# Optimization experiments

Hardware: AMD Instinct MI355X
Metric: run time of the kernel (lower is better)

Reference implementation:

```python
import jax, jax.numpy as jnp
import numpy as np

N, K, D, VOCAB = 20000, 32, 128, 100000
NEG = -1e30  # finite large-negative so all-masked rows don't produce NaN softmax


def setup_inputs() -> dict:
    key = jax.random.key(0)
    ks = jax.random.split(key, 10)
    return {
        "nodes": jax.random.randint(ks[0], (N,), 0, VOCAB),
        "neigh_idx": jax.random.randint(ks[1], (N, K), 0, VOCAB),
        "neigh_len": jax.random.randint(ks[2], (N,), 0, K + 1),
        "u2e": jax.random.normal(ks[3], (VOCAB, D), dtype=jnp.float32),
        "W1": jax.random.normal(ks[4], (D, 2 * D), dtype=jnp.float32) * 0.05,
        "b1": jax.random.normal(ks[5], (D,), dtype=jnp.float32) * 0.05,
        "W2": jax.random.normal(ks[6], (D, D), dtype=jnp.float32) * 0.05,
        "b2": jax.random.normal(ks[7], (D,), dtype=jnp.float32) * 0.05,
        "W3": jax.random.normal(ks[8], (1, D), dtype=jnp.float32) * 0.05,
        "b3": jax.random.normal(ks[9], (1,), dtype=jnp.float32) * 0.05,
    }


def reference(nodes, neigh_idx, neigh_len, u2e, W1, b1, W2, b2, W3, b3):
    # self features: [N, D]
    self_feats = u2e[nodes]
    # neighbor features gather: [N, K, D]
    e_u = u2e[neigh_idx]
    # GraphRec Attention: cat(neighbor, self-broadcast) -> MLP -> softmax over K
    x = jnp.concatenate(
        [e_u, jnp.broadcast_to(self_feats[:, None, :], e_u.shape)], axis=-1
    )  # [N, K, 2D]
    h = jax.nn.relu(jnp.einsum("nkf,df->nkd", x, W1) + b1)
    h = jax.nn.relu(jnp.einsum("nkd,ed->nke", h, W2) + b2)
    logits = jnp.einsum("nkd,od->nko", h, W3)[..., 0] + b3[0]  # [N, K]
    mask = jnp.arange(K)[None, :] < neigh_len[:, None]  # [N, K]
    att = jax.nn.softmax(jnp.where(mask, logits, NEG), axis=1)
    att = jnp.where(mask, att, 0.0)  # zero out padded slots (and all-empty rows)
    # attention-weighted neighbor aggregation: [N, D]
    agg = jnp.einsum("nk,nkd->nd", att, e_u)
    has_neigh = (neigh_len > 0)[:, None]
    return jnp.where(has_neigh, (agg + self_feats) * 0.5, self_feats)
```

## Files before the change

kernel.cpp:

```cpp
#include <hip/hip_runtime.h>
#include <hip/hip_bf16.h>
#include <stdint.h>

#define KN 32
#define D  128
#define NNODES 20000
#define GRID 2500
#define ITERS 4
#define VOCAB 100000
#define CONV_BLOCKS (VOCAB * D / 2048)

typedef __bf16 bf16;
typedef __bf16 bf16x8 __attribute__((ext_vector_type(8)));
typedef float  f32x4  __attribute__((ext_vector_type(4)));

#define CHUNK_E 520
#define EU_NODE_E (8 * CHUNK_E)
#define H_STRIDE 136

#define GL2LDS(src, dst) __builtin_amdgcn_global_load_lds(                 \
    (const __attribute__((address_space(1))) void*)(src),                  \
    (__attribute__((address_space(3))) void*)(dst), 16, 0, 0)

#define MFMA(a, b, c) __builtin_amdgcn_mfma_f32_16x16x32_bf16((a), (b), (c), 0, 0, 0)

__global__ __launch_bounds__(256) void pack_weights_kernel(
    const float* __restrict__ W1, const float* __restrict__ W2,
    bf16* __restrict__ w1p, bf16* __restrict__ w2p)
{
    int t = blockIdx.x * 256 + threadIdx.x;
    if (t < 32768) {
        int j = t & 7, lane = (t >> 3) & 63, kt = (t >> 9) & 7, nt = t >> 12;
        int d = nt * 16 + (lane & 15);
        int f = kt * 32 + ((lane >> 4) << 3) + j;
        w1p[t] = (bf16)W1[d * 256 + f];
    } else if (t < 49152) {
        int u = t - 32768;
        int j = u & 7, lane = (u >> 3) & 63, kt = (u >> 9) & 3, nt = u >> 11;
        int e  = nt * 16 + (lane & 15);
        int dd = kt * 32 + ((lane >> 4) << 3) + j;
        w2p[u] = (bf16)W2[e * 128 + dd];
    }
}

__global__ __launch_bounds__(256) void prep_kernel(
    const float* __restrict__ u2e, const float* __restrict__ W1,
    const float* __restrict__ W2,
    bf16* __restrict__ tbl, bf16* __restrict__ w1p, bf16* __restrict__ w2p)
{
    int b = blockIdx.x;
    if (b < CONV_BLOCKS) {
        size_t i = ((size_t)b * 256 + threadIdx.x) * 8;
        float4 a = *(const float4*)(u2e + i);
        float4 c = *(const float4*)(u2e + i + 4);
        bf16x8 v;
        v[0]=(bf16)a.x; v[1]=(bf16)a.y; v[2]=(bf16)a.z; v[3]=(bf16)a.w;
        v[4]=(bf16)c.x; v[5]=(bf16)c.y; v[6]=(bf16)c.z; v[7]=(bf16)c.w;
        *(bf16x8*)(tbl + i) = v;
    } else {
        int t = (b - CONV_BLOCKS) * 256 + threadIdx.x;
        if (t < 32768) {
            int j = t & 7, lane = (t >> 3) & 63, kt = (t >> 9) & 7, nt = t >> 12;
            int d = nt * 16 + (lane & 15);
            int f = kt * 32 + ((lane >> 4) << 3) + j;
            w1p[t] = (bf16)W1[d * 256 + f];
        } else if (t < 49152) {
            int u = t - 32768;
            int j = u & 7, lane = (u >> 3) & 63, kt = (u >> 9) & 3, nt = u >> 11;
            int e  = nt * 16 + (lane & 15);
            int dd = kt * 32 + ((lane >> 4) << 3) + j;
            w2p[u] = (bf16)W2[e * 128 + dd];
        }
    }
}

__global__ __launch_bounds__(256, 4) void graphrec_agg_kernel(
    const int*   __restrict__ nodes,
    const int*   __restrict__ neigh_idx,
    const int*   __restrict__ neigh_len,
    const float* __restrict__ u2e,
    const bf16*  __restrict__ u2e_bf,
    const float* __restrict__ b1,
    const float* __restrict__ b2,
    const float* __restrict__ W3,
    const float* __restrict__ b3,
    const bf16*  __restrict__ w1p,
    const bf16*  __restrict__ w2p,
    float*       __restrict__ out)
{
    __shared__ alignas(16) bf16  eu[2 * EU_NODE_E];
    __shared__ alignas(16) float self_f[2 * D];
    __shared__ alignas(16) bf16  h1[2 * KN * H_STRIDE];
    __shared__ float lpart[2][4 * KN];

    const int t    = threadIdx.x;
    const int lane = t & 63;
    const int wave = t >> 6;
    const int ln15 = lane & 15;
    const int quad = lane >> 4;
    const int nt0  = wave * 2;

    const float bias1_0 = b1[nt0 * 16 + ln15];
    const float bias1_1 = b1[(nt0 + 1) * 16 + ln15];
    const float bias2_0 = b2[nt0 * 16 + ln15];
    const float bias2_1 = b2[(nt0 + 1) * 16 + ln15];
    const float w3_0    = W3[nt0 * 16 + ln15];
    const float w3_1    = W3[(nt0 + 1) * 16 + ln15];
    const float b3v     = b3[0];

    f32x4 cs0 = {0.f,0.f,0.f,0.f}, cs1 = cs0;
    {
        int nid = nodes[blockIdx.x * 8 + (ln15 & 7)];
        #pragma unroll
        for (int kt = 0; kt < 4; ++kt) {
            bf16x8 a   = *(const bf16x8*)(u2e_bf + (size_t)nid * D + kt * 32 + quad * 8);
            bf16x8 bb0 = *(const bf16x8*)(w1p + (nt0 * 8 + 4 + kt) * 512 + lane * 8);
            bf16x8 bb1 = *(const bf16x8*)(w1p + ((nt0 + 1) * 8 + 4 + kt) * 512 + lane * 8);
            cs0 = MFMA(a, bb0, cs0);
            cs1 = MFMA(a, bb1, cs1);
        }
    }

    bf16x8 w1r[2][4];
    #pragma unroll
    for (int nt = 0; nt < 2; ++nt)
        #pragma unroll
        for (int ft = 0; ft < 4; ++ft)
            w1r[nt][ft] = *(const bf16x8*)(w1p + ((nt0 + nt) * 8 + ft) * 512 + lane * 8);
    bf16x8 w2r[2][4];
    #pragma unroll
    for (int nt = 0; nt < 2; ++nt)
        #pragma unroll
        for (int kt = 0; kt < 4; ++kt)
            w2r[nt][kt] = *(const bf16x8*)(w2p + ((nt0 + nt) * 4 + kt) * 512 + lane * 8);

    #pragma unroll 1
    for (int it = 0; it < ITERS; ++it) {
        const int nA   = blockIdx.x * 8 + it * 2;
        const int lenA = neigh_len[nA];
        const int lenB = neigh_len[nA + 1];

        {
            const int gnd = wave >> 1;
            const int cb  = (wave & 1) * 4;
            #pragma unroll
            for (int j = 0; j < 4; ++j) {
                int chunk = cb + j;
                int idx = neigh_idx[(nA + gnd) * KN + chunk + ((lane >> 4) << 3)];
                GL2LDS(u2e_bf + (size_t)idx * D + ((lane & 15) << 3),
                       eu + gnd * EU_NODE_E + chunk * CHUNK_E);
            }
            if (wave == 0) {
                int sidx = nodes[nA + (lane >> 5)];
                GL2LDS(u2e + (size_t)sidx * D + ((lane & 31) << 2), self_f);
            }
        }
        __syncthreads();

        const bool hi = (it & 1);
        const float selA0 = hi ? cs0[2] : cs0[0];
        const float selB0 = hi ? cs0[3] : cs0[1];
        const float selA1 = hi ? cs1[2] : cs1[0];
        const float selB1 = hi ? cs1[3] : cs1[1];
        const int   srcl  = ((it >> 1) << 4) + ln15;
        const float svA0 = __shfl(selA0, srcl);
        const float svB0 = __shfl(selB0, srcl);
        const float svA1 = __shfl(selA1, srcl);
        const float svB1 = __shfl(selB1, srcl);

        #pragma unroll 1
        for (int nd = 0; nd < 2; ++nd) {
            const bf16* euN = eu + nd * EU_NODE_E;
            bf16* h1N = h1 + nd * KN * H_STRIDE;

            f32x4 c00 = {0.f,0.f,0.f,0.f}, c01 = c00, c10 = c00, c11 = c00;
            const int rb = (ln15 & 7) * CHUNK_E + (ln15 >> 3) * 128;
            #pragma unroll
            for (int ft = 0; ft < 4; ++ft) {
                bf16x8 a0 = *(const bf16x8*)(euN + rb + ft * 32 + quad * 8);
                bf16x8 a1 = *(const bf16x8*)(euN + rb + 256 + ft * 32 + quad * 8);
                c00 = MFMA(a0, w1r[0][ft], c00);
                c01 = MFMA(a0, w1r[1][ft], c01);
                c10 = MFMA(a1, w1r[0][ft], c10);
                c11 = MFMA(a1, w1r[1][ft], c11);
            }
            const float s0 = nd ? svB0 : svA0;
            const float s1 = nd ? svB1 : svA1;
            #pragma unroll
            for (int r = 0; r < 4; ++r) {
                int row = quad * 4 + r;
                h1N[row * H_STRIDE + nt0 * 16 + ln15]              = (bf16)fmaxf(c00[r] + bias1_0 + s0, 0.f);
                h1N[row * H_STRIDE + (nt0 + 1) * 16 + ln15]        = (bf16)fmaxf(c01[r] + bias1_1 + s1, 0.f);
                h1N[(16 + row) * H_STRIDE + nt0 * 16 + ln15]       = (bf16)fmaxf(c10[r] + bias1_0 + s0, 0.f);
                h1N[(16 + row) * H_STRIDE + (nt0 + 1) * 16 + ln15] = (bf16)fmaxf(c11[r] + bias1_1 + s1, 0.f);
            }
        }
        __syncthreads();

        #pragma unroll 1
        for (int nd = 0; nd < 2; ++nd) {
            const bf16* h1N = h1 + nd * KN * H_STRIDE;
            f32x4 d00 = {0.f,0.f,0.f,0.f}, d01 = d00, d10 = d00, d11 = d00;
            #pragma unroll
            for (int kt = 0; kt < 4; ++kt) {
                bf16x8 a0 = *(const bf16x8*)(h1N + ln15 * H_STRIDE + kt * 32 + quad * 8);
                bf16x8 a1 = *(const bf16x8*)(h1N + (16 + ln15) * H_STRIDE + kt * 32 + quad * 8);
                d00 = MFMA(a0, w2r[0][kt], d00);
                d01 = MFMA(a0, w2r[1][kt], d01);
                d10 = MFMA(a1, w2r[0][kt], d10);
                d11 = MFMA(a1, w2r[1][kt], d11);
            }
            #pragma unroll
            for (int r = 0; r < 4; ++r) {
                float p0 = w3_0 * fmaxf(d00[r] + bias2_0, 0.f)
                         + w3_1 * fmaxf(d01[r] + bias2_1, 0.f);
                float p1 = w3_0 * fmaxf(d10[r] + bias2_0, 0.f)
                         + w3_1 * fmaxf(d11[r] + bias2_1, 0.f);
                #pragma unroll
                for (int o = 1; o < 16; o <<= 1) {
                    p0 += __shfl_xor(p0, o);
                    p1 += __shfl_xor(p1, o);
                }
                if (ln15 == 0) {
                    lpart[nd][wave * KN + quad * 4 + r]      = p0;
                    lpart[nd][wave * KN + 16 + quad * 4 + r] = p1;
                }
            }
        }
        __syncthreads();

        {
            const int nd = wave >> 1;
            const int k  = lane & 31;
            float lg = lpart[nd][k] + lpart[nd][KN + k] + lpart[nd][2 * KN + k]
                     + lpart[nd][3 * KN + k] + b3v;
            const int len = nd ? lenB : lenA;
            bool act = k < len;
            float l = act ? lg : -1e30f;
            float m = l;
            #pragma unroll
            for (int o = 1; o < 32; o <<= 1) m = fmaxf(m, __shfl_xor(m, o));
            float e = act ? expf(l - m) : 0.f;
            float s = e;
            #pragma unroll
            for (int o = 1; o < 32; o <<= 1) s += __shfl_xor(s, o);
            float att = (s > 0.f) ? (e / s) : 0.f;

            const int d = ((wave & 1) << 6) + lane;
            const bf16* euN = eu + nd * EU_NODE_E;
            float acc = 0.f;
            #pragma unroll
            for (int k2 = 0; k2 < KN; ++k2) {
                float a  = __shfl(att, k2);
                float ev = (float)euN[(k2 & 7) * CHUNK_E + (k2 >> 3) * 128 + (d & 127)];
                acc += a * ev;
            }
            float sf = self_f[nd * D + (d & 127)];
            out[(size_t)(nA + nd) * D + (d & 127)] = (len > 0) ? 0.5f * (acc + sf) : sf;
        }
        __syncthreads();
    }
}

#define FB_CHUNK_DW 260
#define FB_EU_NODE_DW (16 * FB_CHUNK_DW)

__global__ __launch_bounds__(256, 3) void graphrec_agg_fb(
    const int*   __restrict__ nodes,
    const int*   __restrict__ neigh_idx,
    const int*   __restrict__ neigh_len,
    const float* __restrict__ u2e,
    const float* __restrict__ b1,
    const float* __restrict__ b2,
    const float* __restrict__ W3,
    const float* __restrict__ b3,
    const bf16*  __restrict__ w1p,
    const bf16*  __restrict__ w2p,
    float*       __restrict__ out)
{
    __shared__ alignas(16) float eu[2 * FB_EU_NODE_DW];
    __shared__ alignas(16) bf16  h1[2 * KN * H_STRIDE];
    __shared__ alignas(16) float self_f[2 * D];
    __shared__ float lpart[2][4 * KN];
    __shared__ float att_s[2][KN];

    const int t    = threadIdx.x;
    const int lane = t & 63;
    const int wave = t >> 6;
    const int ln15 = lane & 15;
    const int quad = lane >> 4;
    const int nt0  = wave * 2;

    const float bias1_0 = b1[nt0 * 16 + ln15];
    const float bias1_1 = b1[(nt0 + 1) * 16 + ln15];
    const float bias2_0 = b2[nt0 * 16 + ln15];
    const float bias2_1 = b2[(nt0 + 1) * 16 + ln15];
    const float w3_0    = W3[nt0 * 16 + ln15];
    const float w3_1    = W3[(nt0 + 1) * 16 + ln15];
    const float b3v     = b3[0];

    bf16x8 w1r[2][8];
    #pragma unroll
    for (int nt = 0; nt < 2; ++nt)
        #pragma unroll
        for (int ft = 0; ft < 8; ++ft)
            w1r[nt][ft] = *(const bf16x8*)(w1p + ((nt0 + nt) * 8 + ft) * 512 + lane * 8);
    bf16x8 w2r[2][4];
    #pragma unroll
    for (int nt = 0; nt < 2; ++nt)
        #pragma unroll
        for (int kt = 0; kt < 4; ++kt)
            w2r[nt][kt] = *(const bf16x8*)(w2p + ((nt0 + nt) * 4 + kt) * 512 + lane * 8);

    #pragma unroll 1
    for (int it = 0; it < 4; ++it) {
        const int nA   = blockIdx.x * 8 + it * 2;
        const int lenA = neigh_len[nA];
        const int lenB = neigh_len[nA + 1];
        {
            const int half = lane >> 5;
            const int colb = (lane & 31) << 4;
            #pragma unroll
            for (int nd = 0; nd < 2; ++nd) {
                #pragma unroll
                for (int j = 0; j < 4; ++j) {
                    int chunk = wave * 4 + j;
                    int idx = neigh_idx[(nA + nd) * KN + chunk + (half << 4)];
                    const char* src = (const char*)(u2e + (size_t)idx * D) + colb;
                    GL2LDS(src, eu + nd * FB_EU_NODE_DW + chunk * FB_CHUNK_DW);
                }
            }
            if (wave == 0) {
                int sidx = nodes[nA + half];
                const char* src = (const char*)(u2e + (size_t)sidx * D) + colb;
                GL2LDS(src, self_f);
            }
        }
        __syncthreads();
        #pragma unroll 1
        for (int nd = 0; nd < 2; ++nd) {
            const float* euN = eu + nd * FB_EU_NODE_DW;
            const float* sfN = self_f + nd * D;
            bf16* h1N = h1 + nd * KN * H_STRIDE;
            f32x4 c00 = {0.f,0.f,0.f,0.f}, c01 = c00, c10 = c00, c11 = c00;
            const int r0 = ln15 * FB_CHUNK_DW;
            #pragma unroll
            for (int ft = 0; ft < 4; ++ft) {
                int off = ft * 32 + quad * 8;
                f32x4 u0 = *(const f32x4*)(euN + r0 + off);
                f32x4 u1 = *(const f32x4*)(euN + r0 + off + 4);
                f32x4 v0 = *(const f32x4*)(euN + r0 + 128 + off);
                f32x4 v1 = *(const f32x4*)(euN + r0 + 128 + off + 4);
                bf16x8 a0, a1;
                #pragma unroll
                for (int e = 0; e < 4; ++e) {
                    a0[e] = (bf16)u0[e]; a0[4 + e] = (bf16)u1[e];
                    a1[e] = (bf16)v0[e]; a1[4 + e] = (bf16)v1[e];
                }
                c00 = MFMA(a0, w1r[0][ft], c00);
                c01 = MFMA(a0, w1r[1][ft], c01);
                c10 = MFMA(a1, w1r[0][ft], c10);
                c11 = MFMA(a1, w1r[1][ft], c11);
            }
            #pragma unroll
            for (int ft = 4; ft < 8; ++ft) {
                int off = (ft - 4) * 32 + quad * 8;
                f32x4 u0 = *(const f32x4*)(sfN + off);
                f32x4 u1 = *(const f32x4*)(sfN + off + 4);
                bf16x8 a;
                #pragma unroll
                for (int e = 0; e < 4; ++e) { a[e] = (bf16)u0[e]; a[4 + e] = (bf16)u1[e]; }
                c00 = MFMA(a, w1r[0][ft], c00);
                c01 = MFMA(a, w1r[1][ft], c01);
                c10 = MFMA(a, w1r[0][ft], c10);
                c11 = MFMA(a, w1r[1][ft], c11);
            }
            #pragma unroll
            for (int r = 0; r < 4; ++r) {
                int row = quad * 4 + r;
                h1N[row * H_STRIDE + nt0 * 16 + ln15]              = (bf16)fmaxf(c00[r] + bias1_0, 0.f);
                h1N[row * H_STRIDE + (nt0 + 1) * 16 + ln15]        = (bf16)fmaxf(c01[r] + bias1_1, 0.f);
                h1N[(16 + row) * H_STRIDE + nt0 * 16 + ln15]       = (bf16)fmaxf(c10[r] + bias1_0, 0.f);
                h1N[(16 + row) * H_STRIDE + (nt0 + 1) * 16 + ln15] = (bf16)fmaxf(c11[r] + bias1_1, 0.f);
            }
        }
        __syncthreads();
        #pragma unroll 1
        for (int nd = 0; nd < 2; ++nd) {
            const bf16* h1N = h1 + nd * KN * H_STRIDE;
            f32x4 d00 = {0.f,0.f,0.f,0.f}, d01 = d00, d10 = d00, d11 = d00;
            #pragma unroll
            for (int kt = 0; kt < 4; ++kt) {
                bf16x8 a0 = *(const bf16x8*)(h1N + ln15 * H_STRIDE + kt * 32 + quad * 8);
                bf16x8 a1 = *(const bf16x8*)(h1N + (16 + ln15) * H_STRIDE + kt * 32 + quad * 8);
                d00 = MFMA(a0, w2r[0][kt], d00);
                d01 = MFMA(a0, w2r[1][kt], d01);
                d10 = MFMA(a1, w2r[0][kt], d10);
                d11 = MFMA(a1, w2r[1][kt], d11);
            }
            #pragma unroll
            for (int r = 0; r < 4; ++r) {
                float p0 = w3_0 * fmaxf(d00[r] + bias2_0, 0.f)
                         + w3_1 * fmaxf(d01[r] + bias2_1, 0.f);
                float p1 = w3_0 * fmaxf(d10[r] + bias2_0, 0.f)
                         + w3_1 * fmaxf(d11[r] + bias2_1, 0.f);
                #pragma unroll
                for (int o = 1; o < 16; o <<= 1) {
                    p0 += __shfl_xor(p0, o);
                    p1 += __shfl_xor(p1, o);
                }
                if (ln15 == 0) {
                    lpart[nd][wave * KN + quad * 4 + r]      = p0;
                    lpart[nd][wave * KN + 16 + quad * 4 + r] = p1;
                }
            }
        }
        __syncthreads();
        if (wave < 2) {
            int nd = wave, k = lane & 31;
            float lg = lpart[nd][k] + lpart[nd][KN + k] + lpart[nd][2 * KN + k]
                     + lpart[nd][3 * KN + k] + b3v;
            int len = nd ? lenB : lenA;
            bool act = (lane < 32) && (k < len);
            float l = act ? lg : -1e30f;
            float m = l;
            #pragma unroll
            for (int o = 1; o < 32; o <<= 1) m = fmaxf(m, __shfl_xor(m, o));
            float e = act ? expf(l - m) : 0.f;
            float s = e;
            #pragma unroll
            for (int o = 1; o < 32; o <<= 1) s += __shfl_xor(s, o);
            if (lane < 32) att_s[nd][k] = (s > 0.f) ? (e / s) : 0.f;
        }
        __syncthreads();
        {
            int nd = t >> 7, d = t & 127;
            const float* euN = eu + nd * FB_EU_NODE_DW;
            float acc = 0.f;
            #pragma unroll
            for (int k = 0; k < KN; ++k)
                acc += att_s[nd][k] * euN[(k & 15) * FB_CHUNK_DW + ((k >> 4) << 7) + d];
            float sf = self_f[nd * D + d];
            int len = nd ? lenB : lenA;
            out[(size_t)(nA + nd) * D + d] = (len > 0) ? 0.5f * (acc + sf) : sf;
        }
        __syncthreads();
    }
}

extern "C" void kernel_launch(void* const* d_in, const int* in_sizes, int n_in,
                              void* d_out, int out_size, void* d_ws, size_t ws_size,
                              hipStream_t stream) {
    const int*   nodes     = (const int*)d_in[0];
    const int*   neigh_idx = (const int*)d_in[1];
    const int*   neigh_len = (const int*)d_in[2];
    const float* u2e       = (const float*)d_in[3];
    const float* W1        = (const float*)d_in[4];
    const float* b1        = (const float*)d_in[5];
    const float* W2        = (const float*)d_in[6];
    const float* b2        = (const float*)d_in[7];
    const float* W3        = (const float*)d_in[8];
    const float* b3        = (const float*)d_in[9];
    float* out = (float*)d_out;

    bf16*  w1p    = (bf16*)d_ws;
    bf16*  w2p    = w1p + 32768;
    bf16*  u2e_bf = (bf16*)((char*)d_ws + 98304);
    const size_t need = 98304ull + (size_t)VOCAB * D * 2;

    if (ws_size >= need) {
        prep_kernel<<<CONV_BLOCKS + 192, 256, 0, stream>>>(u2e, W1, W2,
                                                           u2e_bf, w1p, w2p);
        graphrec_agg_kernel<<<GRID, 256, 0, stream>>>(nodes, neigh_idx, neigh_len,
                                                      u2e, u2e_bf, b1, b2,
                                                      W3, b3, w1p, w2p, out);
    } else {
        pack_weights_kernel<<<192, 256, 0, stream>>>(W1, W2, w1p, w2p);
        graphrec_agg_fb<<<GRID, 256, 0, stream>>>(nodes, neigh_idx, neigh_len, u2e,
                                                  b1, b2, W3, b3, w1p, w2p, out);
    }
}
```

Before: 216.1 us.

## Drop bf16 table prep pass; gather fp32 rows and convert inline

Removes the prep kernel that converted the whole 100000x128 embedding table to bf16 and repacked the weights each call. The main kernel now gathers fp32 neighbor rows into registers, converts them to bf16 and writes them to LDS, and builds weight fragments straight from fp32 W1/W2. This avoids reading and writing the full table when only about 640K rows are gathered. The cost is twice the bytes per gathered row, register staging instead of direct global-to-LDS loads, and per-block weight conversion.

```diff
diff --git a/kernel.cpp b/kernel.cpp
--- a/kernel.cpp
+++ b/kernel.cpp
@@ -8,7 +8,6 @@
 #define GRID 2500
 #define ITERS 4
 #define VOCAB 100000
-#define CONV_BLOCKS (VOCAB * D / 2048)
 
 typedef __bf16 bf16;
 typedef __bf16 bf16x8 __attribute__((ext_vector_type(8)));
@@ -24,54 +23,13 @@
 
 #define MFMA(a, b, c) __builtin_amdgcn_mfma_f32_16x16x32_bf16((a), (b), (c), 0, 0, 0)
 
-__global__ __launch_bounds__(256) void pack_weights_kernel(
-    const float* __restrict__ W1, const float* __restrict__ W2,
-    bf16* __restrict__ w1p, bf16* __restrict__ w2p)
-{
-    int t = blockIdx.x * 256 + threadIdx.x;
-    if (t < 32768) {
-        int j = t & 7, lane = (t >> 3) & 63, kt = (t >> 9) & 7, nt = t >> 12;
-        int d = nt * 16 + (lane & 15);
-        int f = kt * 32 + ((lane >> 4) << 3) + j;
-        w1p[t] = (bf16)W1[d * 256 + f];
-    } else if (t < 49152) {
-        int u = t - 32768;
-        int j = u & 7, lane = (u >> 3) & 63, kt = (u >> 9) & 3, nt = u >> 11;
-        int e  = nt * 16 + (lane & 15);
-        int dd = kt * 32 + ((lane >> 4) << 3) + j;
-        w2p[u] = (bf16)W2[e * 128 + dd];
-    }
-}
-
-__global__ __launch_bounds__(256) void prep_kernel(
-    const float* __restrict__ u2e, const float* __restrict__ W1,
-    const float* __restrict__ W2,
-    bf16* __restrict__ tbl, bf16* __restrict__ w1p, bf16* __restrict__ w2p)
-{
-    int b = blockIdx.x;
-    if (b < CONV_BLOCKS) {
-        size_t i = ((size_t)b * 256 + threadIdx.x) * 8;
-        float4 a = *(const float4*)(u2e + i);
-        float4 c = *(const float4*)(u2e + i + 4);
-        bf16x8 v;
-        v[0]=(bf16)a.x; v[1]=(bf16)a.y; v[2]=(bf16)a.z; v[3]=(bf16)a.w;
-        v[4]=(bf16)c.x; v[5]=(bf16)c.y; v[6]=(bf16)c.z; v[7]=(bf16)c.w;
-        *(bf16x8*)(tbl + i) = v;
-    } else {
-        int t = (b - CONV_BLOCKS) * 256 + threadIdx.x;
-        if (t < 32768) {
-            int j = t & 7, lane = (t >> 3) & 63, kt = (t >> 9) & 7, nt = t >> 12;
-            int d = nt * 16 + (lane & 15);
-            int f = kt * 32 + ((lane >> 4) << 3) + j;
-            w1p[t] = (bf16)W1[d * 256 + f];
-        } else if (t < 49152) {
-            int u = t - 32768;
-            int j = u & 7, lane = (u >> 3) & 63, kt = (u >> 9) & 3, nt = u >> 11;
-            int e  = nt * 16 + (lane & 15);
-            int dd = kt * 32 + ((lane >> 4) << 3) + j;
-            w2p[u] = (bf16)W2[e * 128 + dd];
-        }
-    }
+__device__ __forceinline__ bf16x8 frag_from_f32(const float* __restrict__ p) {
+    float4 u0 = *(const float4*)(p);
+    float4 u1 = *(const float4*)(p + 4);
+    bf16x8 a;
+    a[0]=(bf16)u0.x; a[1]=(bf16)u0.y; a[2]=(bf16)u0.z; a[3]=(bf16)u0.w;
+    a[4]=(bf16)u1.x; a[5]=(bf16)u1.y; a[6]=(bf16)u1.z; a[7]=(bf16)u1.w;
+    return a;
 }
 
 __global__ __launch_bounds__(256, 4) void graphrec_agg_kernel(
@@ -79,13 +37,12 @@
     const int*   __restrict__ neigh_idx,
     const int*   __restrict__ neigh_len,
     const float* __restrict__ u2e,
-    const bf16*  __restrict__ u2e_bf,
+    const float* __restrict__ W1,
     const float* __restrict__ b1,
+    const float* __restrict__ W2,
     const float* __restrict__ b2,
     const float* __restrict__ W3,
     const float* __restrict__ b3,
-    const bf16*  __restrict__ w1p,
-    const bf16*  __restrict__ w2p,
     float*       __restrict__ out)
 {
     __shared__ alignas(16) bf16  eu[2 * EU_NODE_E];
@@ -108,31 +65,33 @@
     const float w3_1    = W3[(nt0 + 1) * 16 + ln15];
     const float b3v     = b3[0];
 
+    const size_t w1rowA = (size_t)(nt0 * 16 + ln15) * 256;
+    const size_t w1rowB = (size_t)((nt0 + 1) * 16 + ln15) * 256;
+    const size_t w2rowA = (size_t)(nt0 * 16 + ln15) * 128;
+    const size_t w2rowB = (size_t)((nt0 + 1) * 16 + ln15) * 128;
+    const int    kofs   = quad * 8;
+
     f32x4 cs0 = {0.f,0.f,0.f,0.f}, cs1 = cs0;
     {
         int nid = nodes[blockIdx.x * 8 + (ln15 & 7)];
         #pragma unroll
         for (int kt = 0; kt < 4; ++kt) {
-            bf16x8 a   = *(const bf16x8*)(u2e_bf + (size_t)nid * D + kt * 32 + quad * 8);
-            bf16x8 bb0 = *(const bf16x8*)(w1p + (nt0 * 8 + 4 + kt) * 512 + lane * 8);
-            bf16x8 bb1 = *(const bf16x8*)(w1p + ((nt0 + 1) * 8 + 4 + kt) * 512 + lane * 8);
+            bf16x8 a   = frag_from_f32(u2e + (size_t)nid * D + kt * 32 + kofs);
+            bf16x8 bb0 = frag_from_f32(W1 + w1rowA + 128 + kt * 32 + kofs);
+            bf16x8 bb1 = frag_from_f32(W1 + w1rowB + 128 + kt * 32 + kofs);
             cs0 = MFMA(a, bb0, cs0);
             cs1 = MFMA(a, bb1, cs1);
         }
     }
 
-    bf16x8 w1r[2][4];
+    bf16x8 w1r[2][4], w2r[2][4];
     #pragma unroll
-    for (int nt = 0; nt < 2; ++nt)
-        #pragma unroll
-        for (int ft = 0; ft < 4; ++ft)
-            w1r[nt][ft] = *(const bf16x8*)(w1p + ((nt0 + nt) * 8 + ft) * 512 + lane * 8);
-    bf16x8 w2r[2][4];
-    #pragma unroll
-    for (int nt = 0; nt < 2; ++nt)
-        #pragma unroll
-        for (int kt = 0; kt < 4; ++kt)
-            w2r[nt][kt] = *(const bf16x8*)(w2p + ((nt0 + nt) * 4 + kt) * 512 + lane * 8);
+    for (int ft = 0; ft < 4; ++ft) {
+        w1r[0][ft] = frag_from_f32(W1 + w1rowA + ft * 32 + kofs);
+        w1r[1][ft] = frag_from_f32(W1 + w1rowB + ft * 32 + kofs);
+        w2r[0][ft] = frag_from_f32(W2 + w2rowA + ft * 32 + kofs);
+        w2r[1][ft] = frag_from_f32(W2 + w2rowB + ft * 32 + kofs);
+    }
 
     #pragma unroll 1
     for (int it = 0; it < ITERS; ++it) {
@@ -143,16 +102,29 @@
         {
             const int gnd = wave >> 1;
             const int cb  = (wave & 1) * 4;
-            #pragma unroll
-            for (int j = 0; j < 4; ++j) {
-                int chunk = cb + j;
-                int idx = neigh_idx[(nA + gnd) * KN + chunk + ((lane >> 4) << 3)];
-                GL2LDS(u2e_bf + (size_t)idx * D + ((lane & 15) << 3),
-                       eu + gnd * EU_NODE_E + chunk * CHUNK_E);
+            int4 idx4 = *(const int4*)(neigh_idx + (size_t)(nA + gnd) * KN + cb + (quad << 3));
+            const size_t col = (size_t)(ln15 << 3);
+            float4 v0[4], v1[4];
+            {
+                const float* s0 = u2e + (size_t)idx4.x * D + col;
+                const float* s1 = u2e + (size_t)idx4.y * D + col;
+                const float* s2 = u2e + (size_t)idx4.z * D + col;
+                const float* s3 = u2e + (size_t)idx4.w * D + col;
+                v0[0] = *(const float4*)(s0); v1[0] = *(const float4*)(s0 + 4);
+                v0[1] = *(const float4*)(s1); v1[1] = *(const float4*)(s1 + 4);
+                v0[2] = *(const float4*)(s2); v1[2] = *(const float4*)(s2 + 4);
+                v0[3] = *(const float4*)(s3); v1[3] = *(const float4*)(s3 + 4);
             }
             if (wave == 0) {
                 int sidx = nodes[nA + (lane >> 5)];
                 GL2LDS(u2e + (size_t)sidx * D + ((lane & 31) << 2), self_f);
+            }
+            #pragma unroll
+            for (int j = 0; j < 4; ++j) {
+                bf16x8 w;
+                w[0]=(bf16)v0[j].x; w[1]=(bf16)v0[j].y; w[2]=(bf16)v0[j].z; w[3]=(bf16)v0[j].w;
+                w[4]=(bf16)v1[j].x; w[5]=(bf16)v1[j].y; w[6]=(bf16)v1[j].z; w[7]=(bf16)v1[j].w;
+                *(bf16x8*)(eu + gnd * EU_NODE_E + (cb + j) * CHUNK_E + quad * 128 + ln15 * 8) = w;
             }
         }
         __syncthreads();
@@ -262,192 +234,6 @@
     }
 }
 
-#define FB_CHUNK_DW 260
-#define FB_EU_NODE_DW (16 * FB_CHUNK_DW)
-
-__global__ __launch_bounds__(256, 3) void graphrec_agg_fb(
-    const int*   __restrict__ nodes,
-    const int*   __restrict__ neigh_idx,
-    const int*   __restrict__ neigh_len,
-    const float* __restrict__ u2e,
-    const float* __restrict__ b1,
-    const float* __restrict__ b2,
-    const float* __restrict__ W3,
-    const float* __restrict__ b3,
-    const bf16*  __restrict__ w1p,
-    const bf16*  __restrict__ w2p,
-    float*       __restrict__ out)
-{
-    __shared__ alignas(16) float eu[2 * FB_EU_NODE_DW];
-    __shared__ alignas(16) bf16  h1[2 * KN * H_STRIDE];
-    __shared__ alignas(16) float self_f[2 * D];
-    __shared__ float lpart[2][4 * KN];
-    __shared__ float att_s[2][KN];
-
-    const int t    = threadIdx.x;
-    const int lane = t & 63;
-    const int wave = t >> 6;
-    const int ln15 = lane & 15;
-    const int quad = lane >> 4;
-    const int nt0  = wave * 2;
-
-    const float bias1_0 = b1[nt0 * 16 + ln15];
-    const float bias1_1 = b1[(nt0 + 1) * 16 + ln15];
-    const float bias2_0 = b2[nt0 * 16 + ln15];
-    const float bias2_1 = b2[(nt0 + 1) * 16 + ln15];
-    const float w3_0    = W3[nt0 * 16 + ln15];
-    const float w3_1    = W3[(nt0 + 1) * 16 + ln15];
-    const float b3v     = b3[0];
-
-    bf16x8 w1r[2][8];
-    #pragma unroll
-    for (int nt = 0; nt < 2; ++nt)
-        #pragma unroll
-        for (int ft = 0; ft < 8; ++ft)
-            w1r[nt][ft] = *(const bf16x8*)(w1p + ((nt0 + nt) * 8 + ft) * 512 + lane * 8);
-    bf16x8 w2r[2][4];
-    #pragma unroll
-    for (int nt = 0; nt < 2; ++nt)
-        #pragma unroll
-        for (int kt = 0; kt < 4; ++kt)
-            w2r[nt][kt] = *(const bf16x8*)(w2p + ((nt0 + nt) * 4 + kt) * 512 + lane * 8);
-
-    #pragma unroll 1
-    for (int it = 0; it < 4; ++it) {
-        const int nA   = blockIdx.x * 8 + it * 2;
-        const int lenA = neigh_len[nA];
-        const int lenB = neigh_len[nA + 1];
-        {
-            const int half = lane >> 5;
-            const int colb = (lane & 31) << 4;
-            #pragma unroll
-            for (int nd = 0; nd < 2; ++nd) {
-                #pragma unroll
-                for (int j = 0; j < 4; ++j) {
-                    int chunk = wave * 4 + j;
-                    int idx = neigh_idx[(nA + nd) * KN + chunk + (half << 4)];
-                    const char* src = (const char*)(u2e + (size_t)idx * D) + colb;
-                    GL2LDS(src, eu + nd * FB_EU_NODE_DW + chunk * FB_CHUNK_DW);
-                }
-            }
-            if (wave == 0) {
-                int sidx = nodes[nA + half];
-                const char* src = (const char*)(u2e + (size_t)sidx * D) + colb;
-                GL2LDS(src, self_f);
-            }
-        }
-        __syncthreads();
-        #pragma unroll 1
-        for (int nd = 0; nd < 2; ++nd) {
-            const float* euN = eu + nd * FB_EU_NODE_DW;
-            const float* sfN = self_f + nd * D;
-            bf16* h1N = h1 + nd * KN * H_STRIDE;
-            f32x4 c00 = {0.f,0.f,0.f,0.f}, c01 = c00, c10 = c00, c11 = c00;
-            const int r0 = ln15 * FB_CHUNK_DW;
-            #pragma unroll
-            for (int ft = 0; ft < 4; ++ft) {
-                int off = ft * 32 + quad * 8;
-                f32x4 u0 = *(const f32x4*)(euN + r0 + off);
-                f32x4 u1 = *(const f32x4*)(euN + r0 + off + 4);
-                f32x4 v0 = *(const f32x4*)(euN + r0 + 128 + off);
-                f32x4 v1 = *(const f32x4*)(euN + r0 + 128 + off + 4);
-                bf16x8 a0, a1;
-                #pragma unroll
-                for (int e = 0; e < 4; ++e) {
-                    a0[e] = (bf16)u0[e]; a0[4 + e] = (bf16)u1[e];
-                    a1[e] = (bf16)v0[e]; a1[4 + e] = (bf16)v1[e];
-                }
-                c00 = MFMA(a0, w1r[0][ft], c00);
-                c01 = MFMA(a0, w1r[1][ft], c01);
-                c10 = MFMA(a1, w1r[0][ft], c10);
-                c11 = MFMA(a1, w1r[1][ft], c11);
-            }
-            #pragma unroll
-            for (int ft = 4; ft < 8; ++ft) {
-                int off = (ft - 4) * 32 + quad * 8;
-                f32x4 u0 = *(const f32x4*)(sfN + off);
-                f32x4 u1 = *(const f32x4*)(sfN + off + 4);
-                bf16x8 a;
-                #pragma unroll
-                for (int e = 0; e < 4; ++e) { a[e] = (bf16)u0[e]; a[4 + e] = (bf16)u1[e]; }
-                c00 = MFMA(a, w1r[0][ft], c00);
-                c01 = MFMA(a, w1r[1][ft], c01);
-                c10 = MFMA(a, w1r[0][ft], c10);
-                c11 = MFMA(a, w1r[1][ft], c11);
-            }
-            #pragma unroll
-            for (int r = 0; r < 4; ++r) {
-                int row = quad * 4 + r;
-                h1N[row * H_STRIDE + nt0 * 16 + ln15]              = (bf16)fmaxf(c00[r] + bias1_0, 0.f);
-                h1N[row * H_STRIDE + (nt0 + 1) * 16 + ln15]        = (bf16)fmaxf(c01[r] + bias1_1, 0.f);
-                h1N[(16 + row) * H_STRIDE + nt0 * 16 + ln15]       = (bf16)fmaxf(c10[r] + bias1_0, 0.f);
-                h1N[(16 + row) * H_STRIDE + (nt0 + 1) * 16 + ln15] = (bf16)fmaxf(c11[r] + bias1_1, 0.f);
-            }
-        }
-        __syncthreads();
-        #pragma unroll 1
-        for (int nd = 0; nd < 2; ++nd) {
-            const bf16* h1N = h1 + nd * KN * H_STRIDE;
-            f32x4 d00 = {0.f,0.f,0.f,0.f}, d01 = d00, d10 = d00, d11 = d00;
-            #pragma unroll
-            for (int kt = 0; kt < 4; ++kt) {
-                bf16x8 a0 = *(const bf16x8*)(h1N + ln15 * H_STRIDE + kt * 32 + quad * 8);
-                bf16x8 a1 = *(const bf16x8*)(h1N + (16 + ln15) * H_STRIDE + kt * 32 + quad * 8);
-                d00 = MFMA(a0, w2r[0][kt], d00);
-                d01 = MFMA(a0, w2r[1][kt], d01);
-                d10 = MFMA(a1, w2r[0][kt], d10);
-                d11 = MFMA(a1, w2r[1][kt], d11);
-            }
-            #pragma unroll
-            for (int r = 0; r < 4; ++r) {
-                float p0 = w3_0 * fmaxf(d00[r] + bias2_0, 0.f)
-                         + w3_1 * fmaxf(d01[r] + bias2_1, 0.f);
-                float p1 = w3_0 * fmaxf(d10[r] + bias2_0, 0.f)
-                         + w3_1 * fmaxf(d11[r] + bias2_1, 0.f);
-                #pragma unroll
-                for (int o = 1; o < 16; o <<= 1) {
-                    p0 += __shfl_xor(p0, o);
-                    p1 += __shfl_xor(p1, o);
-                }
-                if (ln15 == 0) {
-                    lpart[nd][wave * KN + quad * 4 + r]      = p0;
-                    lpart[nd][wave * KN + 16 + quad * 4 + r] = p1;
-                }
-            }
-        }
-        __syncthreads();
-        if (wave < 2) {
-            int nd = wave, k = lane & 31;
-            float lg = lpart[nd][k] + lpart[nd][KN + k] + lpart[nd][2 * KN + k]
-                     + lpart[nd][3 * KN + k] + b3v;
-            int len = nd ? lenB : lenA;
-            bool act = (lane < 32) && (k < len);
-            float l = act ? lg : -1e30f;
-            float m = l;
-            #pragma unroll
-            for (int o = 1; o < 32; o <<= 1) m = fmaxf(m, __shfl_xor(m, o));
-            float e = act ? expf(l - m) : 0.f;
-            float s = e;
-            #pragma unroll
-            for (int o = 1; o < 32; o <<= 1) s += __shfl_xor(s, o);
-            if (lane < 32) att_s[nd][k] = (s > 0.f) ? (e / s) : 0.f;
-        }
-        __syncthreads();
-        {
-            int nd = t >> 7, d = t & 127;
-            const float* euN = eu + nd * FB_EU_NODE_DW;
-            float acc = 0.f;
-            #pragma unroll
-            for (int k = 0; k < KN; ++k)
-                acc += att_s[nd][k] * euN[(k & 15) * FB_CHUNK_DW + ((k >> 4) << 7) + d];
-            float sf = self_f[nd * D + d];
-            int len = nd ? lenB : lenA;
-            out[(size_t)(nA + nd) * D + d] = (len > 0) ? 0.5f * (acc + sf) : sf;
-        }
-        __syncthreads();
-    }
-}
-
 extern "C" void kernel_launch(void* const* d_in, const int* in_sizes, int n_in,
                               void* d_out, int out_size, void* d_ws, size_t ws_size,
                               hipStream_t stream) {
@@ -462,21 +248,9 @@
     const float* W3        = (const float*)d_in[8];
     const float* b3        = (const float*)d_in[9];
     float* out = (float*)d_out;
-
-    bf16*  w1p    = (bf16*)d_ws;
-    bf16*  w2p    = w1p + 32768;
-    bf16*  u2e_bf = (bf16*)((char*)d_ws + 98304);
-    const size_t need = 98304ull + (size_t)VOCAB * D * 2;
-
-    if (ws_size >= need) {
-        prep_kernel<<<CONV_BLOCKS + 192, 256, 0, stream>>>(u2e, W1, W2,
-                                                           u2e_bf, w1p, w2p);
-        graphrec_agg_kernel<<<GRID, 256, 0, stream>>>(nodes, neigh_idx, neigh_len,
-                                                      u2e, u2e_bf, b1, b2,
-                                                      W3, b3, w1p, w2p, out);
-    } else {
-        pack_weights_kernel<<<192, 256, 0, stream>>>(W1, W2, w1p, w2p);
-        graphrec_agg_fb<<<GRID, 256, 0, stream>>>(nodes, neigh_idx, neigh_len, u2e,
-                                                  b1, b2, W3, b3, w1p, w2p, out);
-    }
+    (void)d_ws; (void)ws_size; (void)in_sizes; (void)n_in; (void)out_size;
+
+    graphrec_agg_kernel<<<GRID, 256, 0, stream>>>(nodes, neigh_idx, neigh_len,
+                                                  u2e, W1, b1, W2, b2, W3, b3,
+                                                  out);
 }
```

Result: slower. 266.3 us (+23.2%).
